# Kernel optimization log

Measured on AMD Instinct MI355X. Metric: run time of the kernel, lower is better.

The kernel has to match this reference:

```python
import jax, jax.numpy as jnp
import numpy as np

VOCAB, EMBED, ZCH = 4096, 128, 256
B, H, W = 32, 16, 16


def setup_inputs() -> dict:
    key = jax.random.key(0)
    k1, k2, k3, k4 = jax.random.split(key, 4)
    z_e = jax.random.normal(k1, (B, ZCH, H, W), dtype=jnp.float32)
    pre_w = jax.random.normal(k2, (EMBED, ZCH), dtype=jnp.float32) * 0.02
    pre_b = jnp.zeros((EMBED,), dtype=jnp.float32)
    # codebook initialized uniform(-1/vocab, 1/vocab) like the torch module
    emb = jax.random.uniform(k3, (VOCAB, EMBED), dtype=jnp.float32,
                             minval=-1.0 / VOCAB, maxval=1.0 / VOCAB)
    post_w = jax.random.normal(k4, (ZCH, EMBED), dtype=jnp.float32) * 0.02
    post_b = jnp.zeros((ZCH,), dtype=jnp.float32)
    return {"z_e": z_e, "pre_w": pre_w, "pre_b": pre_b, "emb": emb,
            "post_w": post_w, "post_b": post_b}


def reference(z_e, pre_w, pre_b, emb, post_w, post_b):
    # pre_quant_conv: 1x1 conv == per-pixel linear, z_channels -> embed_dim
    z = jnp.einsum('bchw,ec->behw', z_e, pre_w) + pre_b[None, :, None, None]
    b, e, h, w = z.shape
    zf = z.transpose(0, 2, 3, 1).reshape(-1, e)                 # (b*h*w, e)
    # squared distance to all codebook vectors: |z|^2 + |c|^2 - 2 z.c
    dist = (jnp.sum(zf * zf, axis=1, keepdims=True)
            + jnp.sum(emb * emb, axis=1)
            - 2.0 * zf @ emb.T)                                  # (b*h*w, vocab)
    tokens = jnp.argmin(dist, axis=-1)                           # (b*h*w,)
    z_q = emb[tokens].reshape(b, h, w, e).transpose(0, 3, 1, 2)  # (b,e,h,w)
    # straight-through estimator
    dec_in = z + jax.lax.stop_gradient(z_q - z)
    # post_quant_conv: 1x1 conv embed_dim -> z_channels (decoder input)
    rec = jnp.einsum('behw,ce->bchw', dec_in, post_w) + post_b[None, :, None, None]
    return z, z_q, rec
```

## Files before the change

kernel.cpp:

```cpp
#include <hip/hip_runtime.h>
#include <hip/hip_bf16.h>
#include <cstdint>

#define NB   32
#define NC   256
#define NE   128
#define NS   256
#define NV   4096
#define NP   8192
#define NSPLIT 8

typedef unsigned short ushort_t;
typedef __attribute__((ext_vector_type(8))) short bf16x8;
typedef __attribute__((ext_vector_type(8))) unsigned short us8;
typedef __attribute__((ext_vector_type(4))) float f32x4;

__device__ __forceinline__ float bf2f(ushort_t u) {
    union { unsigned int i; float f; } x; x.i = ((unsigned int)u) << 16; return x.f;
}
__device__ __forceinline__ ushort_t f2bf(float f) {
    __hip_bfloat16 h = __float2bfloat16(f);
    ushort_t u; __builtin_memcpy(&u, &h, 2); return u;
}
__device__ __forceinline__ unsigned asu(float f) { unsigned u; __builtin_memcpy(&u,&f,4); return u; }
__device__ __forceinline__ float    asf(unsigned u) { float f; __builtin_memcpy(&f,&u,4); return f; }

__global__ __launch_bounds__(256) void pre_conv_pack(
    const float* __restrict__ z_e, const float* __restrict__ pre_w,
    const float* __restrict__ pre_b, const float* __restrict__ emb,
    float* __restrict__ out_z, ushort_t* __restrict__ Bpack,
    float* __restrict__ cnorm)
{
    __shared__ __align__(16) float wtile[16 * 256];
    __shared__ __align__(16) float part[4 * 16 * 64];

    const int t = threadIdx.x;

    if (blockIdx.x == 8) {
        const int v     = (blockIdx.y * 4 + blockIdx.z) * 32 + (t >> 3);
        const int chunk = t & 7;
        const float4* rp = (const float4*)(emb + (size_t)v * NE + chunk * 16);
        float4 x0 = rp[0], x1 = rp[1], x2 = rp[2], x3 = rp[3];
        float xs[16] = { x0.x, x0.y, x0.z, x0.w, x1.x, x1.y, x1.z, x1.w,
                         x2.x, x2.y, x2.z, x2.w, x3.x, x3.y, x3.z, x3.w };
        us8 h0, h1;
        float nn = 0.f;
#pragma unroll
        for (int j = 0; j < 8; j++) {
            nn = fmaf(xs[j], xs[j], nn);
            h0[j] = f2bf(xs[j]);
        }
#pragma unroll
        for (int j = 0; j < 8; j++) {
            nn = fmaf(xs[8 + j], xs[8 + j], nn);
            h1[j] = f2bf(xs[8 + j]);
        }
        nn += __shfl_xor(nn, 1);
        nn += __shfl_xor(nn, 2);
        nn += __shfl_xor(nn, 4);
        if (chunk == 0) cnorm[v] = 0.5f * nn;

        const int G  = v >> 4;
        const int ks = chunk >> 1;
        const int q0 = (chunk & 1) * 2;
        const int L0 = (v & 15) | (q0 << 4);
        const int L1 = (v & 15) | ((q0 + 1) << 4);
        *(us8*)(Bpack + ((size_t)G * 4 + ks) * 512 + L0 * 8) = h0;
        *(us8*)(Bpack + ((size_t)G * 4 + ks) * 512 + L1 * 8) = h1;
        return;
    }

    const int e0 = blockIdx.x * 16;
    const int b  = blockIdx.y;
    const int s0 = blockIdx.z * 64;

    for (int idx = t; idx < 16 * 256; idx += 256)
        wtile[idx] = pre_w[(e0 + (idx >> 8)) * 256 + (idx & 255)];
    __syncthreads();

    const int kq = t >> 6, sl = t & 63;
    float acc[16];
#pragma unroll
    for (int r = 0; r < 16; r++) acc[r] = 0.f;

    const float* zin = z_e + (size_t)(b * NC + kq * 64) * NS + s0 + sl;
    const int cb = kq * 64;
#pragma unroll 4
    for (int i = 0; i < 16; i++) {
        const int c = i * 4;
        float z0 = zin[(c + 0) * NS];
        float z1 = zin[(c + 1) * NS];
        float z2 = zin[(c + 2) * NS];
        float z3 = zin[(c + 3) * NS];
#pragma unroll
        for (int r = 0; r < 16; r++) {
            float4 w = *(const float4*)&wtile[r * 256 + cb + c];
            acc[r] = fmaf(z0, w.x, fmaf(z1, w.y, fmaf(z2, w.z, fmaf(z3, w.w, acc[r]))));
        }
    }
#pragma unroll
    for (int r = 0; r < 16; r++)
        part[(kq * 16 + r) * 64 + sl] = acc[r];
    __syncthreads();

    const int r4 = t >> 6, sl2 = t & 63;
#pragma unroll
    for (int j = 0; j < 4; j++) {
        const int r = j * 4 + r4;
        float v = pre_b[e0 + r]
                + part[(0 * 16 + r) * 64 + sl2]
                + part[(1 * 16 + r) * 64 + sl2]
                + part[(2 * 16 + r) * 64 + sl2]
                + part[(3 * 16 + r) * 64 + sl2];
        out_z[(size_t)(b * NE + e0 + r) * NS + s0 + sl2] = v;
    }
}

__global__ __launch_bounds__(256, 3) void score_mfma(
    const float* __restrict__ z, const ushort_t* __restrict__ Bpack,
    const float* __restrict__ cnorm, int* __restrict__ pidx4)
{
    __shared__ __align__(16) char smraw[40960];
    float* As  = (float*)smraw;
    float* r1  = (float*)smraw;
    float* r2  = (float*)(smraw + 16640);
    float* t4b = (float*)(smraw + 33280);

    const int t = threadIdx.x;
    const int wave = t >> 6, lane = t & 63;
    const int set = blockIdx.x;
    const int split = blockIdx.y;
    const int p0 = set * 64;
    const int b  = p0 >> 8;
    const int s0 = p0 & 255;

    for (int idx = t; idx < 64 * 128; idx += 256) {
        int k = idx >> 6, i = idx & 63;
        As[i * 132 + k] = z[(size_t)(b * NE + k) * NS + s0 + i];
    }
    __syncthreads();

    const int am = lane & 15, aq = lane >> 4;
    bf16x8 ah[4][4];
#pragma unroll
    for (int mt = 0; mt < 4; mt++)
#pragma unroll
        for (int ks = 0; ks < 4; ks++) {
            const unsigned* src = (const unsigned*)(As + (mt * 16 + am) * 132 + ks * 32 + aq * 8);
            union { unsigned u[4]; bf16x8 v; } pk;
#pragma unroll
            for (int pr = 0; pr < 4; pr++)
                pk.u[pr] = (src[2 * pr + 1] & 0xFFFF0000u) | (src[2 * pr] >> 16);
            ah[mt][ks] = pk.v;
        }
    __syncthreads();

    const int Gbase = split * 32 + wave * 8;
    float cn[8];
#pragma unroll
    for (int cgi = 0; cgi < 8; cgi++)
        cn[cgi] = cnorm[(Gbase + cgi) * 16 + am];

    float b1v[16], b2v[16];
#pragma unroll
    for (int i = 0; i < 16; i++) { b1v[i] = -1e30f; b2v[i] = -1e30f; }

    bf16x8 bh[4], bhn[4];
#pragma unroll
    for (int ks = 0; ks < 4; ks++)
        bh[ks] = *(const bf16x8*)(Bpack + ((size_t)Gbase * 4 + ks) * 512 + lane * 8);

    for (int cgi = 0; cgi < 8; cgi++) {
        if (cgi < 7) {
#pragma unroll
            for (int ks = 0; ks < 4; ks++)
                bhn[ks] = *(const bf16x8*)(Bpack + ((size_t)(Gbase + cgi + 1) * 4 + ks) * 512 + lane * 8);
        }

        f32x4 acc[4];
#pragma unroll
        for (int mt = 0; mt < 4; mt++) acc[mt] = (f32x4){0.f, 0.f, 0.f, 0.f};
#pragma unroll
        for (int ks = 0; ks < 4; ks++)
#pragma unroll
            for (int mt = 0; mt < 4; mt++)
                acc[mt] = __builtin_amdgcn_mfma_f32_16x16x32_bf16(ah[mt][ks], bh[ks], acc[mt], 0, 0, 0);

#pragma unroll
        for (int mt = 0; mt < 4; mt++)
#pragma unroll
            for (int reg = 0; reg < 4; reg++) {
                const int si = mt * 4 + reg;
                float sc = acc[mt][reg] - cn[cgi];
                float ev = asf((asu(sc) & ~7u) | (unsigned)cgi);
                b2v[si] = fmaxf(b2v[si], fminf(ev, b1v[si]));
                b1v[si] = fmaxf(b1v[si], ev);
            }
#pragma unroll
        for (int ks = 0; ks < 4; ks++) bh[ks] = bhn[ks];
    }

    const int slot = wave * 16 + am;
#pragma unroll
    for (int mt = 0; mt < 4; mt++)
#pragma unroll
        for (int reg = 0; reg < 4; reg++) {
            int px = mt * 16 + aq * 4 + reg;
            r1[slot * 65 + px] = b1v[mt * 4 + reg];
            r2[slot * 65 + px] = b2v[mt * 4 + reg];
        }
    __syncthreads();

    {
        const int px = t >> 2, ch = t & 3;
        float t1 = -1e30f, t2 = -1e30f, t3 = -1e30f, t4 = -1e30f;
        for (int i = 0; i < 16; i++) {
            int sl = ch * 16 + i;
#pragma unroll
            for (int e = 0; e < 2; e++) {
                float raw = e ? r2[sl * 65 + px] : r1[sl * 65 + px];
                unsigned vb = asu(raw);
                float v = asf((vb & ~511u) | ((unsigned)sl << 3) | (vb & 7u));
                t4 = fmaxf(t4, fminf(v, t3));
                t3 = fmaxf(t3, fminf(v, t2));
                t2 = fmaxf(t2, fminf(v, t1));
                t1 = fmaxf(t1, v);
            }
        }
        float* dst = t4b + (px * 4 + ch) * 4;
        dst[0] = t1; dst[1] = t2; dst[2] = t3; dst[3] = t4;
    }
    __syncthreads();

    if (t < 64) {
        float u1 = -1e30f, u2 = -1e30f, u3 = -1e30f, u4 = -1e30f;
        for (int ch = 0; ch < 4; ch++) {
#pragma unroll
            for (int j = 0; j < 4; j++) {
                float v = t4b[(t * 4 + ch) * 4 + j];
                u4 = fmaxf(u4, fminf(v, u3));
                u3 = fmaxf(u3, fminf(v, u2));
                u2 = fmaxf(u2, fminf(v, u1));
                u1 = fmaxf(u1, v);
            }
        }
        const int p = p0 + t;
        float uu[4] = { u1, u2, u3, u4 };
#pragma unroll
        for (int j = 0; j < 4; j++) {
            unsigned bits = asu(uu[j]) & 511u;
            int w = (int)(bits >> 7), res = (int)((bits >> 3) & 15u), cg = (int)(bits & 7u);
            pidx4[((size_t)split * NP + p) * 4 + j] = split * 512 + (w * 8 + cg) * 16 + res;
        }
    }
}

__global__ __launch_bounds__(256) void rescore_gather_post(
    const float* __restrict__ z, const float* __restrict__ emb,
    const int* __restrict__ pidx4, const float* __restrict__ post_w,
    const float* __restrict__ post_b, float* __restrict__ out_zq,
    float* __restrict__ out_rec)
{
    __shared__ __align__(16) float zl[16 * 132];
    __shared__ double bsl[16 * 16];
    __shared__ int    bil[16 * 16];
    __shared__ int    tok[16];
    __shared__ __align__(16) float eg[16 * 132];
    __shared__ __align__(16) float wtile[64 * 129];
    __shared__ float  outb[64 * 17];

    const int t  = threadIdx.x;
    const int p0 = blockIdx.x * 16;
    const int b  = p0 >> 8;
    const int s0 = p0 & 255;

    for (int idx = t; idx < 16 * 128; idx += 256) {
        int k = idx >> 4, i = idx & 15;
        zl[i * 132 + k] = z[(size_t)(b * NE + k) * NS + s0 + i];
    }
    __syncthreads();

    const int il = t >> 4;
    const int cc = t & 15;
    const int p  = p0 + il;
    double bs = -1e300; int bi = 0x7fffffff;
#pragma unroll
    for (int jj = 0; jj < 2; jj++) {
        int cand = cc * 2 + jj;
        int split = cand >> 2, slot = cand & 3;
        int idx = pidx4[((size_t)split * NP + p) * 4 + slot];
        const float* er = emb + (size_t)idx * NE;
        double dot = 0.0, nn = 0.0;
        for (int k = 0; k < NE; k += 4) {
            float4 e4 = *(const float4*)(er + k);
            dot += (double)zl[il * 132 + k + 0] * (double)e4.x;
            dot += (double)zl[il * 132 + k + 1] * (double)e4.y;
            dot += (double)zl[il * 132 + k + 2] * (double)e4.z;
            dot += (double)zl[il * 132 + k + 3] * (double)e4.w;
            nn  += (double)e4.x * e4.x + (double)e4.y * e4.y
                 + (double)e4.z * e4.z + (double)e4.w * e4.w;
        }
        double sc = dot - 0.5 * nn;
        if (sc > bs || (sc == bs && idx < bi)) { bs = sc; bi = idx; }
    }
    bsl[il * 16 + cc] = bs;
    bil[il * 16 + cc] = bi;
    __syncthreads();

    if (t < 16) {
        double B = -1e300; int I = 0x7fffffff;
        for (int c = 0; c < 16; c++) {
            double sc = bsl[t * 16 + c]; int ii = bil[t * 16 + c];
            if (sc > B || (sc == B && ii < I)) { B = sc; I = ii; }
        }
        tok[t] = I;
    }
    __syncthreads();

    for (int idx = t; idx < NE * 16; idx += 256) {
        int e = idx >> 4, i = idx & 15;
        float v = emb[(size_t)tok[i] * NE + e];
        out_zq[(size_t)(b * NE + e) * NS + s0 + i] = v;
        eg[i * 132 + e] = v;
    }
    __syncthreads();

    const int pg  = t >> 6;
    const int cl  = t & 63;
    const int px0 = pg * 4;
    const float* g0 = &eg[(px0 + 0) * 132];
    const float* g1 = &eg[(px0 + 1) * 132];
    const float* g2 = &eg[(px0 + 2) * 132];
    const float* g3 = &eg[(px0 + 3) * 132];

    for (int ct = 0; ct < 4; ct++) {
        for (int idx = t; idx < 64 * 128; idx += 256) {
            int r = idx >> 7, k = idx & 127;
            wtile[r * 129 + k] = post_w[(size_t)(ct * 64 + r) * 128 + k];
        }
        __syncthreads();

        float a0 = 0.f, a1 = 0.f, a2 = 0.f, a3 = 0.f;
        const float* wr = &wtile[cl * 129];
#pragma unroll 4
        for (int k = 0; k < 128; k += 4) {
            float w0 = wr[k + 0], w1 = wr[k + 1], w2 = wr[k + 2], w3 = wr[k + 3];
            float4 q0 = *(const float4*)&g0[k];
            float4 q1 = *(const float4*)&g1[k];
            float4 q2 = *(const float4*)&g2[k];
            float4 q3 = *(const float4*)&g3[k];
            a0 = fmaf(w0, q0.x, fmaf(w1, q0.y, fmaf(w2, q0.z, fmaf(w3, q0.w, a0))));
            a1 = fmaf(w0, q1.x, fmaf(w1, q1.y, fmaf(w2, q1.z, fmaf(w3, q1.w, a1))));
            a2 = fmaf(w0, q2.x, fmaf(w1, q2.y, fmaf(w2, q2.z, fmaf(w3, q2.w, a2))));
            a3 = fmaf(w0, q3.x, fmaf(w1, q3.y, fmaf(w2, q3.z, fmaf(w3, q3.w, a3))));
        }
        float bias = post_b[ct * 64 + cl];
        outb[cl * 17 + px0 + 0] = a0 + bias;
        outb[cl * 17 + px0 + 1] = a1 + bias;
        outb[cl * 17 + px0 + 2] = a2 + bias;
        outb[cl * 17 + px0 + 3] = a3 + bias;
        __syncthreads();

        for (int idx = t; idx < 64 * 16; idx += 256) {
            int c_loc = idx >> 4, px = idx & 15;
            out_rec[(size_t)(b * NC + ct * 64 + c_loc) * NS + s0 + px] =
                outb[c_loc * 17 + px];
        }
        __syncthreads();
    }
}

extern "C" void kernel_launch(void* const* d_in, const int* in_sizes, int n_in,
                              void* d_out, int out_size, void* d_ws, size_t ws_size,
                              hipStream_t stream)
{
    const float* z_e    = (const float*)d_in[0];
    const float* pre_w  = (const float*)d_in[1];
    const float* pre_b  = (const float*)d_in[2];
    const float* emb    = (const float*)d_in[3];
    const float* post_w = (const float*)d_in[4];
    const float* post_b = (const float*)d_in[5];

    float* out     = (float*)d_out;
    float* out_z   = out;
    float* out_zq  = out + 1048576;
    float* out_rec = out + 2097152;

    const size_t SZ_BPACK = (size_t)256 * 4 * 512 * 2;
    const size_t SZ_CNORM = (size_t)NV * 4;
    const size_t SZ_PIDX4 = (size_t)NSPLIT * NP * 4 * 4;
    const size_t NEED = SZ_BPACK + SZ_CNORM + SZ_PIDX4;
    char* scr = (ws_size >= NEED) ? (char*)d_ws : (char*)out_rec;
    ushort_t* Bpack = (ushort_t*)scr;
    float*    cnorm = (float*)(scr + SZ_BPACK);
    int*      pidx4 = (int*)(scr + SZ_BPACK + SZ_CNORM);

    pre_conv_pack      <<<dim3(9, 32, 4),    256, 0, stream>>>(z_e, pre_w, pre_b, emb,
                                                               out_z, Bpack, cnorm);
    score_mfma         <<<dim3(128, NSPLIT), 256, 0, stream>>>(out_z, Bpack, cnorm, pidx4);
    rescore_gather_post<<<dim3(512),         256, 0, stream>>>(out_z, emb, pidx4,
                                                               post_w, post_b,
                                                               out_zq, out_rec);
}
```

Baseline: 158.6 us.

## Rework rescore kernel: 512 threads, shuffle argmin, direct-global post conv

The final rescore/gather/post-conv kernel now uses 512 threads, so each of 32 lanes per pixel rescores one candidate, and the best candidate is picked with a wavefront xor-shuffle reduction instead of shared-memory passes and extra barriers. The double-precision dot products use four independent accumulators to shorten dependency chains. The post conv drops the shared weight tile and staging buffer: each thread reads one post_w row directly from global/cache and computes 8 pixels, writing float4 outputs. This cuts LDS traffic and synchronisation but relies on cache for weight reuse and changes the FP64 summation order.

```diff
diff --git a/kernel.cpp b/kernel.cpp
--- a/kernel.cpp
+++ b/kernel.cpp
@@ -255,69 +255,78 @@
     }
 }
 
-__global__ __launch_bounds__(256) void rescore_gather_post(
+__global__ __launch_bounds__(512, 4) void rescore_gather_post2(
     const float* __restrict__ z, const float* __restrict__ emb,
     const int* __restrict__ pidx4, const float* __restrict__ post_w,
     const float* __restrict__ post_b, float* __restrict__ out_zq,
     float* __restrict__ out_rec)
 {
     __shared__ __align__(16) float zl[16 * 132];
-    __shared__ double bsl[16 * 16];
-    __shared__ int    bil[16 * 16];
-    __shared__ int    tok[16];
     __shared__ __align__(16) float eg[16 * 132];
-    __shared__ __align__(16) float wtile[64 * 129];
-    __shared__ float  outb[64 * 17];
+    __shared__ int tok[16];
 
     const int t  = threadIdx.x;
     const int p0 = blockIdx.x * 16;
     const int b  = p0 >> 8;
     const int s0 = p0 & 255;
 
-    for (int idx = t; idx < 16 * 128; idx += 256) {
+    for (int idx = t; idx < 16 * 128; idx += 512) {
         int k = idx >> 4, i = idx & 15;
         zl[i * 132 + k] = z[(size_t)(b * NE + k) * NS + s0 + i];
     }
     __syncthreads();
 
-    const int il = t >> 4;
-    const int cc = t & 15;
-    const int p  = p0 + il;
-    double bs = -1e300; int bi = 0x7fffffff;
-#pragma unroll
-    for (int jj = 0; jj < 2; jj++) {
-        int cand = cc * 2 + jj;
-        int split = cand >> 2, slot = cand & 3;
-        int idx = pidx4[((size_t)split * NP + p) * 4 + slot];
+    {
+        const int il = t >> 5;
+        const int cc = t & 31;
+        const int p  = p0 + il;
+        const int split = cc >> 2, slot = cc & 3;
+        const int idx = pidx4[((size_t)split * NP + p) * 4 + slot];
         const float* er = emb + (size_t)idx * NE;
-        double dot = 0.0, nn = 0.0;
-        for (int k = 0; k < NE; k += 4) {
-            float4 e4 = *(const float4*)(er + k);
-            dot += (double)zl[il * 132 + k + 0] * (double)e4.x;
-            dot += (double)zl[il * 132 + k + 1] * (double)e4.y;
-            dot += (double)zl[il * 132 + k + 2] * (double)e4.z;
-            dot += (double)zl[il * 132 + k + 3] * (double)e4.w;
-            nn  += (double)e4.x * e4.x + (double)e4.y * e4.y
-                 + (double)e4.z * e4.z + (double)e4.w * e4.w;
-        }
-        double sc = dot - 0.5 * nn;
-        if (sc > bs || (sc == bs && idx < bi)) { bs = sc; bi = idx; }
-    }
-    bsl[il * 16 + cc] = bs;
-    bil[il * 16 + cc] = bi;
-    __syncthreads();
-
-    if (t < 16) {
-        double B = -1e300; int I = 0x7fffffff;
-        for (int c = 0; c < 16; c++) {
-            double sc = bsl[t * 16 + c]; int ii = bil[t * 16 + c];
-            if (sc > B || (sc == B && ii < I)) { B = sc; I = ii; }
-        }
-        tok[t] = I;
-    }
-    __syncthreads();
-
-    for (int idx = t; idx < NE * 16; idx += 256) {
+        const float* zr = &zl[il * 132];
+
+        double d0 = 0.0, d1 = 0.0, d2 = 0.0, d3 = 0.0;
+        double n0 = 0.0, n1 = 0.0, n2 = 0.0, n3 = 0.0;
+#pragma unroll
+        for (int k = 0; k < NE; k += 16) {
+            float4 e0 = *(const float4*)(er + k + 0);
+            float4 e1 = *(const float4*)(er + k + 4);
+            float4 e2 = *(const float4*)(er + k + 8);
+            float4 e3 = *(const float4*)(er + k + 12);
+            float4 z0 = *(const float4*)(zr + k + 0);
+            float4 z1 = *(const float4*)(zr + k + 4);
+            float4 z2 = *(const float4*)(zr + k + 8);
+            float4 z3 = *(const float4*)(zr + k + 12);
+            d0 += (double)z0.x * e0.x; d0 += (double)z0.y * e0.y;
+            d0 += (double)z0.z * e0.z; d0 += (double)z0.w * e0.w;
+            d1 += (double)z1.x * e1.x; d1 += (double)z1.y * e1.y;
+            d1 += (double)z1.z * e1.z; d1 += (double)z1.w * e1.w;
+            d2 += (double)z2.x * e2.x; d2 += (double)z2.y * e2.y;
+            d2 += (double)z2.z * e2.z; d2 += (double)z2.w * e2.w;
+            d3 += (double)z3.x * e3.x; d3 += (double)z3.y * e3.y;
+            d3 += (double)z3.z * e3.z; d3 += (double)z3.w * e3.w;
+            n0 += (double)e0.x * e0.x; n0 += (double)e0.y * e0.y;
+            n0 += (double)e0.z * e0.z; n0 += (double)e0.w * e0.w;
+            n1 += (double)e1.x * e1.x; n1 += (double)e1.y * e1.y;
+            n1 += (double)e1.z * e1.z; n1 += (double)e1.w * e1.w;
+            n2 += (double)e2.x * e2.x; n2 += (double)e2.y * e2.y;
+            n2 += (double)e2.z * e2.z; n2 += (double)e2.w * e2.w;
+            n3 += (double)e3.x * e3.x; n3 += (double)e3.y * e3.y;
+            n3 += (double)e3.z * e3.z; n3 += (double)e3.w * e3.w;
+        }
+        double bs = ((d0 + d1) + (d2 + d3)) - 0.5 * ((n0 + n1) + (n2 + n3));
+        int bi = idx;
+#pragma unroll
+        for (int m = 1; m <= 16; m <<= 1) {
+            double osc = __shfl_xor(bs, m);
+            int    obi = __shfl_xor(bi, m);
+            if (osc > bs || (osc == bs && obi < bi)) { bs = osc; bi = obi; }
+        }
+        if (cc == 0) tok[il] = bi;
+    }
+    __syncthreads();
+
+    for (int idx = t; idx < NE * 16; idx += 512) {
         int e = idx >> 4, i = idx & 15;
         float v = emb[(size_t)tok[i] * NE + e];
         out_zq[(size_t)(b * NE + e) * NS + s0 + i] = v;
@@ -325,48 +334,41 @@
     }
     __syncthreads();
 
-    const int pg  = t >> 6;
-    const int cl  = t & 63;
-    const int px0 = pg * 4;
-    const float* g0 = &eg[(px0 + 0) * 132];
-    const float* g1 = &eg[(px0 + 1) * 132];
-    const float* g2 = &eg[(px0 + 2) * 132];
-    const float* g3 = &eg[(px0 + 3) * 132];
-
-    for (int ct = 0; ct < 4; ct++) {
-        for (int idx = t; idx < 64 * 128; idx += 256) {
-            int r = idx >> 7, k = idx & 127;
-            wtile[r * 129 + k] = post_w[(size_t)(ct * 64 + r) * 128 + k];
-        }
-        __syncthreads();
+    {
+        const int c  = t & 255;
+        const int ph = t >> 8;
+        const int pb = ph * 8;
+        const float* wr = post_w + (size_t)c * NE;
 
         float a0 = 0.f, a1 = 0.f, a2 = 0.f, a3 = 0.f;
-        const float* wr = &wtile[cl * 129];
+        float a4 = 0.f, a5 = 0.f, a6 = 0.f, a7 = 0.f;
 #pragma unroll 4
-        for (int k = 0; k < 128; k += 4) {
-            float w0 = wr[k + 0], w1 = wr[k + 1], w2 = wr[k + 2], w3 = wr[k + 3];
-            float4 q0 = *(const float4*)&g0[k];
-            float4 q1 = *(const float4*)&g1[k];
-            float4 q2 = *(const float4*)&g2[k];
-            float4 q3 = *(const float4*)&g3[k];
-            a0 = fmaf(w0, q0.x, fmaf(w1, q0.y, fmaf(w2, q0.z, fmaf(w3, q0.w, a0))));
-            a1 = fmaf(w0, q1.x, fmaf(w1, q1.y, fmaf(w2, q1.z, fmaf(w3, q1.w, a1))));
-            a2 = fmaf(w0, q2.x, fmaf(w1, q2.y, fmaf(w2, q2.z, fmaf(w3, q2.w, a2))));
-            a3 = fmaf(w0, q3.x, fmaf(w1, q3.y, fmaf(w2, q3.z, fmaf(w3, q3.w, a3))));
-        }
-        float bias = post_b[ct * 64 + cl];
-        outb[cl * 17 + px0 + 0] = a0 + bias;
-        outb[cl * 17 + px0 + 1] = a1 + bias;
-        outb[cl * 17 + px0 + 2] = a2 + bias;
-        outb[cl * 17 + px0 + 3] = a3 + bias;
-        __syncthreads();
-
-        for (int idx = t; idx < 64 * 16; idx += 256) {
-            int c_loc = idx >> 4, px = idx & 15;
-            out_rec[(size_t)(b * NC + ct * 64 + c_loc) * NS + s0 + px] =
-                outb[c_loc * 17 + px];
-        }
-        __syncthreads();
+        for (int k = 0; k < NE; k += 4) {
+            float4 w4 = *(const float4*)(wr + k);
+            float4 q;
+            q = *(const float4*)&eg[(pb + 0) * 132 + k];
+            a0 = fmaf(w4.x, q.x, fmaf(w4.y, q.y, fmaf(w4.z, q.z, fmaf(w4.w, q.w, a0))));
+            q = *(const float4*)&eg[(pb + 1) * 132 + k];
+            a1 = fmaf(w4.x, q.x, fmaf(w4.y, q.y, fmaf(w4.z, q.z, fmaf(w4.w, q.w, a1))));
+            q = *(const float4*)&eg[(pb + 2) * 132 + k];
+            a2 = fmaf(w4.x, q.x, fmaf(w4.y, q.y, fmaf(w4.z, q.z, fmaf(w4.w, q.w, a2))));
+            q = *(const float4*)&eg[(pb + 3) * 132 + k];
+            a3 = fmaf(w4.x, q.x, fmaf(w4.y, q.y, fmaf(w4.z, q.z, fmaf(w4.w, q.w, a3))));
+            q = *(const float4*)&eg[(pb + 4) * 132 + k];
+            a4 = fmaf(w4.x, q.x, fmaf(w4.y, q.y, fmaf(w4.z, q.z, fmaf(w4.w, q.w, a4))));
+            q = *(const float4*)&eg[(pb + 5) * 132 + k];
+            a5 = fmaf(w4.x, q.x, fmaf(w4.y, q.y, fmaf(w4.z, q.z, fmaf(w4.w, q.w, a5))));
+            q = *(const float4*)&eg[(pb + 6) * 132 + k];
+            a6 = fmaf(w4.x, q.x, fmaf(w4.y, q.y, fmaf(w4.z, q.z, fmaf(w4.w, q.w, a6))));
+            q = *(const float4*)&eg[(pb + 7) * 132 + k];
+            a7 = fmaf(w4.x, q.x, fmaf(w4.y, q.y, fmaf(w4.z, q.z, fmaf(w4.w, q.w, a7))));
+        }
+        const float bias = post_b[c];
+        float4 lo = { a0 + bias, a1 + bias, a2 + bias, a3 + bias };
+        float4 hi = { a4 + bias, a5 + bias, a6 + bias, a7 + bias };
+        float* dst = out_rec + (size_t)(b * NC + c) * NS + s0 + pb;
+        *(float4*)(dst + 0) = lo;
+        *(float4*)(dst + 4) = hi;
     }
 }
 
@@ -395,10 +397,10 @@
     float*    cnorm = (float*)(scr + SZ_BPACK);
     int*      pidx4 = (int*)(scr + SZ_BPACK + SZ_CNORM);
 
-    pre_conv_pack      <<<dim3(9, 32, 4),    256, 0, stream>>>(z_e, pre_w, pre_b, emb,
-                                                               out_z, Bpack, cnorm);
-    score_mfma         <<<dim3(128, NSPLIT), 256, 0, stream>>>(out_z, Bpack, cnorm, pidx4);
-    rescore_gather_post<<<dim3(512),         256, 0, stream>>>(out_z, emb, pidx4,
-                                                               post_w, post_b,
-                                                               out_zq, out_rec);
-}
+    pre_conv_pack       <<<dim3(9, 32, 4),    256, 0, stream>>>(z_e, pre_w, pre_b, emb,
+                                                                out_z, Bpack, cnorm);
+    score_mfma          <<<dim3(128, NSPLIT), 256, 0, stream>>>(out_z, Bpack, cnorm, pidx4);
+    rescore_gather_post2<<<dim3(512),         512, 0, stream>>>(out_z, emb, pidx4,
+                                                                post_w, post_b,
+                                                                out_zq, out_rec);
+}
```

Result: faster. 152.9 us (-3.6%).
